# Kernel optimization log

Measured on AMD Instinct MI355X. Metric: run time of the kernel, lower is better.

## Reference

```python
import jax, jax.numpy as jnp
import numpy as np

N_NODES = 50000
N_EDGES = 1000000
IN_CH = 256
HID_CH = 128
HEADS = 2
OUT_CH = 3
NEG_SLOPE = 0.2  # PyG GATConv default leaky_relu slope


def setup_inputs() -> dict:
    key = jax.random.key(0)
    ks = jax.random.split(key, 10)
    s = 0.1
    x = jax.random.normal(ks[0], (N_NODES, IN_CH), dtype=jnp.float32)
    edge_index = jax.random.randint(ks[1], (2, N_EDGES), 0, N_NODES, dtype=jnp.int64)
    # GATConv layer 1 (heads=2, concat=True)
    W1 = jax.random.normal(ks[2], (IN_CH, HEADS * HID_CH), dtype=jnp.float32) * s
    a_src1 = jax.random.normal(ks[3], (HEADS, HID_CH), dtype=jnp.float32) * s
    a_dst1 = jax.random.normal(ks[4], (HEADS, HID_CH), dtype=jnp.float32) * s
    b1 = jnp.zeros((HEADS * HID_CH,), dtype=jnp.float32)
    # GATConv layer 2 (heads=1, concat=False)
    W2 = jax.random.normal(ks[5], (HEADS * HID_CH, OUT_CH), dtype=jnp.float32) * s
    a_src2 = jax.random.normal(ks[6], (1, OUT_CH), dtype=jnp.float32) * s
    a_dst2 = jax.random.normal(ks[7], (1, OUT_CH), dtype=jnp.float32) * s
    b2 = jnp.zeros((OUT_CH,), dtype=jnp.float32)
    return dict(x=x, edge_index=edge_index, W1=W1, a_src1=a_src1, a_dst1=a_dst1,
                b1=b1, W2=W2, a_src2=a_src2, a_dst2=a_dst2, b2=b2)


def gat_layer(x, edge_index, W, a_src, a_dst, b, concat):
    # x: [N, F_in]; W: [F_in, H*C]; a_src/a_dst: [H, C]
    n = x.shape[0]
    H, C = a_src.shape
    h = (x @ W).reshape(n, H, C)                       # [N, H, C]
    al_s = jnp.einsum('nhc,hc->nh', h, a_src)          # [N, H]
    al_d = jnp.einsum('nhc,hc->nh', h, a_dst)          # [N, H]
    src, dst = edge_index[0], edge_index[1]
    e = jax.nn.leaky_relu(al_s[src] + al_d[dst], NEG_SLOPE)   # [E, H]
    # segment softmax over incoming edges of each dst node
    e_max = jax.ops.segment_max(e, dst, num_segments=n)       # [N, H]
    w = jnp.exp(e - e_max[dst])                                # [E, H]
    denom = jax.ops.segment_sum(w, dst, num_segments=n)        # [N, H]
    alpha = w / jnp.maximum(denom[dst], 1e-16)                 # [E, H]
    out = jax.ops.segment_sum(h[src] * alpha[:, :, None], dst, num_segments=n)  # [N, H, C]
    out = out.reshape(n, H * C) if concat else out.mean(axis=1)
    return out + b


def reference(x, edge_index, W1, a_src1, a_dst1, b1, W2, a_src2, a_dst2, b2):
    # dropout(p=0.6) is identity in eval mode
    h = jax.nn.elu(gat_layer(x, edge_index, W1, a_src1, a_dst1, b1, concat=True))
    h = gat_layer(h, edge_index, W2, a_src2, a_dst2, b2, concat=False)
    return jax.nn.log_softmax(h, axis=1)
```

## Files before the change

### kernel.cpp

```cpp
#include <hip/hip_runtime.h>

#define N_NODES 50000
#define N_EDGES 1000000
#define FIN 256
#define F1  256
#define OUTC 3
#define BUCKET 64
#define GEMM_BLOCKS ((N_NODES + 63) / 64)
#define EDGE_BLOCKS ((N_EDGES + 255) / 256)

typedef __attribute__((ext_vector_type(8))) short  short8;
typedef __attribute__((ext_vector_type(4))) float  f32x4;
typedef __attribute__((ext_vector_type(2))) float  f32x2;

__device__ __forceinline__ unsigned short f2bf(float f) {
  unsigned int x; __builtin_memcpy(&x, &f, 4);
  x += 0x7fffu + ((x >> 16) & 1u);
  return (unsigned short)(x >> 16);
}
__device__ __forceinline__ float u2f(unsigned int x) {
  float f; __builtin_memcpy(&f, &x, 4); return f;
}
__device__ __forceinline__ float wredmax(float v) {
  #pragma unroll
  for (int m = 32; m > 0; m >>= 1) v = fmaxf(v, __shfl_xor(v, m));
  return v;
}
__device__ __forceinline__ float wredsum(float v) {
  #pragma unroll
  for (int m = 32; m > 0; m >>= 1) v += __shfl_xor(v, m);
  return v;
}

__global__ __launch_bounds__(256) void k_t(const float* __restrict__ w1,
                                           unsigned short* __restrict__ w1t,
                                           int* __restrict__ deg) {
  int idx = blockIdx.x * 256 + threadIdx.x;
  int k = idx >> 8, n = idx & 255;
  w1t[n * 256 + k] = f2bf(w1[k * 256 + n]);
  if (idx < N_NODES) deg[idx] = 0;
}

__global__ __launch_bounds__(256) void k_bg(
    const float* __restrict__ x,
    const unsigned short* __restrict__ w1t,
    const float* __restrict__ a_src1,
    const float* __restrict__ a_dst1,
    unsigned short* __restrict__ h1b,
    float* __restrict__ als1,
    float* __restrict__ ald1,
    const int* __restrict__ ei,
    int* __restrict__ deg, unsigned short* __restrict__ bucket) {
  const int t = threadIdx.x;

  if (blockIdx.x >= GEMM_BLOCKS) {
    __shared__ int sflag;
    if (t < 64) {
      int idx = 2 * (t * 15625 + 7) + 1;
      unsigned long long b = __ballot(ei[idx] != 0);
      if (t == 0) sflag = (b != 0ull) ? 1 : 0;
    }
    __syncthreads();
    const int f = sflag;
    int e = (blockIdx.x - GEMM_BLOCKS) * 256 + t;
    if (e < N_EDGES) {
      int s, d;
      if (f) { s = ei[e];     d = ei[N_EDGES + e]; }
      else   { s = ei[2 * e]; d = ei[2 * (N_EDGES + e)]; }
      int pos = atomicAdd(&deg[d], 1);
      if (pos < BUCKET) bucket[d * BUCKET + pos] = (unsigned short)s;
    }
    return;
  }

  const int wv   = t >> 6;
  const int lane = t & 63;
  const int m    = lane & 15;
  const int quad = lane >> 4;
  const int row0 = blockIdx.x * 64 + wv * 16;

  int arow = row0 + m;
  if (arow > N_NODES - 1) arow = N_NODES - 1;
  const float* xrow = x + (size_t)arow * FIN + quad * 8;

  short8 af[8];
  #pragma unroll
  for (int kk = 0; kk < 8; ++kk) {
    f32x4 v0 = *(const f32x4*)(xrow + kk * 32);
    f32x4 v1 = *(const f32x4*)(xrow + kk * 32 + 4);
    short8 fr;
    #pragma unroll
    for (int j = 0; j < 4; ++j) {
      fr[j]     = (short)f2bf(v0[j]);
      fr[j + 4] = (short)f2bf(v1[j]);
    }
    af[kk] = fr;
  }

  f32x4 acc[16];
  #pragma unroll
  for (int c = 0; c < 16; ++c) {
    const unsigned short* bp = w1t + (size_t)(c * 16 + m) * FIN + quad * 8;
    f32x4 a = {0.f, 0.f, 0.f, 0.f};
    #pragma unroll
    for (int kk = 0; kk < 8; ++kk) {
      short8 bf = *(const short8*)(bp + kk * 32);
      a = __builtin_amdgcn_mfma_f32_16x16x32_bf16(af[kk], bf, a, 0, 0, 0);
    }
    acc[c] = a;
  }

  float s0[4] = {0,0,0,0}, s1[4] = {0,0,0,0}, d0[4] = {0,0,0,0}, d1[4] = {0,0,0,0};
  #pragma unroll
  for (int c = 0; c < 16; ++c) {
    int ch = c * 16 + m;
    float av = a_src1[ch];
    float dv = a_dst1[ch];
    if (c < 8) {
      #pragma unroll
      for (int r = 0; r < 4; ++r) { s0[r] += acc[c][r] * av; d0[r] += acc[c][r] * dv; }
    } else {
      #pragma unroll
      for (int r = 0; r < 4; ++r) { s1[r] += acc[c][r] * av; d1[r] += acc[c][r] * dv; }
    }
  }
  #pragma unroll
  for (int msk = 1; msk < 16; msk <<= 1) {
    #pragma unroll
    for (int r = 0; r < 4; ++r) {
      s0[r] += __shfl_xor(s0[r], msk);
      s1[r] += __shfl_xor(s1[r], msk);
      d0[r] += __shfl_xor(d0[r], msk);
      d1[r] += __shfl_xor(d1[r], msk);
    }
  }
  #pragma unroll
  for (int r = 0; r < 4; ++r) {
    int row = row0 + quad * 4 + r;
    if (row < N_NODES) {
      unsigned short* hrow = h1b + (size_t)row * F1 + m;
      #pragma unroll
      for (int c = 0; c < 16; ++c) hrow[c * 16] = f2bf(acc[c][r]);
      if (m == 0) {
        als1[row * 2 + 0] = s0[r]; als1[row * 2 + 1] = s1[r];
        ald1[row * 2 + 0] = d0[r]; ald1[row * 2 + 1] = d1[r];
      }
    }
  }
}

__global__ __launch_bounds__(256) void k_attn1(
    const unsigned short* __restrict__ bucket,
    const int* __restrict__ deg,
    const float* __restrict__ als1,
    const float* __restrict__ ald1,
    const unsigned short* __restrict__ h1b,
    const float* __restrict__ b1,
    const float* __restrict__ w2,
    const float* __restrict__ a_src2,
    const float* __restrict__ a_dst2,
    float4* __restrict__ h2pack,
    float* __restrict__ ald2) {
  const int wv   = threadIdx.x >> 6;
  const int lane = threadIdx.x & 63;
  const int n = blockIdx.x * 4 + wv;
  if (n >= N_NODES) return;
  const int dg = min(deg[n], BUCKET);
  const float ad0  = ald1[n * 2 + 0];
  const float ad1v = ald1[n * 2 + 1];
  const float2* alsv = (const float2*)als1;

  const int l31   = lane & 31;
  const int ehalf = lane >> 5;
  const bool head1 = (l31 >= 16);

  float l0 = -1e30f, l1 = -1e30f; int sreg = 0;
  if (lane < dg) {
    sreg = (int)bucket[n * BUCKET + lane];
    float2 a = alsv[sreg];
    l0 = a.x + ad0;  l0 = l0 > 0.f ? l0 : 0.2f * l0;
    l1 = a.y + ad1v; l1 = l1 > 0.f ? l1 : 0.2f * l1;
  }
  const float m0 = wredmax(l0), m1 = wredmax(l1);
  const float e0 = (lane < dg) ? __expf(l0 - m0) : 0.f;
  const float e1 = (lane < dg) ? __expf(l1 - m1) : 0.f;
  const float sum0 = wredsum(e0), sum1 = wredsum(e1);
  const float inv = 1.f / fmaxf(head1 ? sum1 : sum0, 1e-16f);

  f32x2 accv[4] = {{0.f,0.f},{0.f,0.f},{0.f,0.f},{0.f,0.f}};
  const int pairs = (dg + 1) >> 1;
  for (int e = 0; e < pairs; e += 4) {
    float w[4]; int sv[4];
    #pragma unroll
    for (int k = 0; k < 4; ++k) {
      int eidx = 2 * (e + k) + ehalf;
      int esel = eidx & 63;
      float w0 = __shfl(e0, esel);
      float w1 = __shfl(e1, esel);
      sv[k] = __shfl(sreg, esel);
      w[k] = head1 ? w1 : w0;
      if (eidx >= dg) w[k] = 0.f;
    }
    uint4 hv[4];
    #pragma unroll
    for (int k = 0; k < 4; ++k)
      hv[k] = *(const uint4*)(h1b + (size_t)sv[k] * F1 + l31 * 8);
    #pragma unroll
    for (int k = 0; k < 4; ++k) {
      const unsigned int* hu = (const unsigned int*)&hv[k];
      f32x2 wv2 = {w[k], w[k]};
      #pragma unroll
      for (int j = 0; j < 4; ++j) {
        unsigned int u = hu[j];
        f32x2 h;
        h.x = u2f(u << 16);
        h.y = u2f(u & 0xffff0000u);
        accv[j] = __builtin_elementwise_fma(wv2, h, accv[j]);
      }
    }
  }

  float* av = (float*)accv;
  #pragma unroll
  for (int j = 0; j < 8; ++j) av[j] += __shfl_xor(av[j], 32);

  float p0 = 0.f, p1 = 0.f, p2 = 0.f;
  #pragma unroll
  for (int j = 0; j < 8; ++j) {
    int ch = l31 * 8 + j;
    float tt = av[j] * inv + b1[ch];
    tt = tt > 0.f ? tt : __expf(tt) - 1.f;
    p0 = fmaf(tt, w2[ch * 3 + 0], p0);
    p1 = fmaf(tt, w2[ch * 3 + 1], p1);
    p2 = fmaf(tt, w2[ch * 3 + 2], p2);
  }
  p0 = wredsum(p0) * 0.5f;
  p1 = wredsum(p1) * 0.5f;
  p2 = wredsum(p2) * 0.5f;
  if (lane == 0) {
    float als2v = p0 * a_src2[0] + p1 * a_src2[1] + p2 * a_src2[2];
    h2pack[n] = make_float4(p0, p1, p2, als2v);
    ald2[n] = p0 * a_dst2[0] + p1 * a_dst2[1] + p2 * a_dst2[2];
  }
}

__global__ __launch_bounds__(256) void k_attn2(
    const unsigned short* __restrict__ bucket,
    const int* __restrict__ deg,
    const float4* __restrict__ h2pack,
    const float* __restrict__ ald2,
    const float* __restrict__ b2,
    float* __restrict__ out) {
  const int wv   = threadIdx.x >> 6;
  const int lane = threadIdx.x & 63;
  const int n = blockIdx.x * 4 + wv;
  if (n >= N_NODES) return;
  const int dg = min(deg[n], BUCKET);
  const float adn = ald2[n];

  float l = -1e30f;
  float4 hp = make_float4(0.f, 0.f, 0.f, 0.f);
  if (lane < dg) {
    int s = (int)bucket[n * BUCKET + lane];
    hp = h2pack[s];
    l = hp.w + adn;
    l = l > 0.f ? l : 0.2f * l;
  }
  const float m = wredmax(l);
  const float e = (lane < dg) ? __expf(l - m) : 0.f;
  const float sum = wredsum(e);
  const float inv = 1.f / fmaxf(sum, 1e-16f);
  float p0 = wredsum(e * hp.x);
  float p1 = wredsum(e * hp.y);
  float p2 = wredsum(e * hp.z);

  if (lane == 0) {
    float o0 = p0 * inv + b2[0];
    float o1 = p1 * inv + b2[1];
    float o2 = p2 * inv + b2[2];
    float mm = fmaxf(o0, fmaxf(o1, o2));
    float ls = logf(__expf(o0 - mm) + __expf(o1 - mm) + __expf(o2 - mm));
    out[n * 3 + 0] = o0 - mm - ls;
    out[n * 3 + 1] = o1 - mm - ls;
    out[n * 3 + 2] = o2 - mm - ls;
  }
}

extern "C" void kernel_launch(void* const* d_in, const int* in_sizes, int n_in,
                              void* d_out, int out_size, void* d_ws, size_t ws_size,
                              hipStream_t stream) {
  (void)in_sizes; (void)n_in; (void)out_size; (void)ws_size;
  const float* x      = (const float*)d_in[0];
  const int*   ei     = (const int*)d_in[1];
  const float* W1     = (const float*)d_in[2];
  const float* a_src1 = (const float*)d_in[3];
  const float* a_dst1 = (const float*)d_in[4];
  const float* b1     = (const float*)d_in[5];
  const float* W2     = (const float*)d_in[6];
  const float* a_src2 = (const float*)d_in[7];
  const float* a_dst2 = (const float*)d_in[8];
  const float* b2     = (const float*)d_in[9];
  float* out = (float*)d_out;

  char* p = (char*)d_ws;
  auto alloc = [&](size_t bytes) -> char* {
    char* r = p; p += (bytes + 511) & ~(size_t)511; return r;
  };
  unsigned short* w1t  = (unsigned short*)alloc(65536ull * 2);
  unsigned short* h1b  = (unsigned short*)alloc((size_t)N_NODES * F1 * 2);
  float*  als1   = (float*)alloc((size_t)N_NODES * 2 * 4);
  float*  ald1   = (float*)alloc((size_t)N_NODES * 2 * 4);
  float4* h2pack = (float4*)alloc((size_t)N_NODES * 16);
  float*  ald2   = (float*)alloc((size_t)N_NODES * 4);
  int*    deg    = (int*)alloc((size_t)N_NODES * 4);
  unsigned short* bucket = (unsigned short*)alloc((size_t)N_NODES * BUCKET * 2);

  hipLaunchKernelGGL(k_t, dim3(256), dim3(256), 0, stream, W1, w1t, deg);
  hipLaunchKernelGGL(k_bg, dim3(GEMM_BLOCKS + EDGE_BLOCKS), dim3(256), 0, stream,
                     x, w1t, a_src1, a_dst1, h1b, als1, ald1, ei, deg, bucket);
  hipLaunchKernelGGL(k_attn1, dim3((N_NODES + 3) / 4), dim3(256), 0, stream,
                     bucket, deg, als1, ald1, h1b, b1, W2, a_src2, a_dst2,
                     h2pack, ald2);
  hipLaunchKernelGGL(k_attn2, dim3((N_NODES + 3) / 4), dim3(256), 0, stream,
                     bucket, deg, h2pack, ald2, b2, out);
}
```

Measured before the change: 252.8 us.

## Stage W1 slices in LDS per block and split GEMM by head

Drops the separate W1 transpose kernel. Each GEMM block now converts its own 128-column half of W1 to bf16 and stages it in shared memory in two K-chunks, then feeds the MFMAs from LDS instead of from global memory. The GEMM grid doubles so that each block handles one head, which halves the per-thread accumulators and the reduction work. The degree array is now zeroed with a memset. In exchange, every block re-reads and re-converts W1 from fp32 global memory and the x rows are loaded twice, adding redundant traffic and barriers.

```diff
diff --git a/kernel.cpp b/kernel.cpp
--- a/kernel.cpp
+++ b/kernel.cpp
@@ -6,8 +6,9 @@
 #define F1  256
 #define OUTC 3
 #define BUCKET 64
-#define GEMM_BLOCKS ((N_NODES + 63) / 64)
+#define GEMM_BLOCKS (((N_NODES + 63) / 64) * 2)
 #define EDGE_BLOCKS ((N_EDGES + 255) / 256)
+#define LDSW 136
 
 typedef __attribute__((ext_vector_type(8))) short  short8;
 typedef __attribute__((ext_vector_type(4))) float  f32x4;
@@ -32,18 +33,9 @@
   return v;
 }
 
-__global__ __launch_bounds__(256) void k_t(const float* __restrict__ w1,
-                                           unsigned short* __restrict__ w1t,
-                                           int* __restrict__ deg) {
-  int idx = blockIdx.x * 256 + threadIdx.x;
-  int k = idx >> 8, n = idx & 255;
-  w1t[n * 256 + k] = f2bf(w1[k * 256 + n]);
-  if (idx < N_NODES) deg[idx] = 0;
-}
-
-__global__ __launch_bounds__(256) void k_bg(
+__global__ __launch_bounds__(256) void k_bg2(
     const float* __restrict__ x,
-    const unsigned short* __restrict__ w1t,
+    const float* __restrict__ w1,
     const float* __restrict__ a_src1,
     const float* __restrict__ a_dst1,
     unsigned short* __restrict__ h1b,
@@ -51,6 +43,7 @@
     float* __restrict__ ald1,
     const int* __restrict__ ei,
     int* __restrict__ deg, unsigned short* __restrict__ bucket) {
+  __shared__ unsigned short lw[128 * LDSW];
   const int t = threadIdx.x;
 
   if (blockIdx.x >= GEMM_BLOCKS) {
@@ -73,11 +66,14 @@
     return;
   }
 
+  const int rb   = blockIdx.x >> 1;
+  const int s    = blockIdx.x & 1;
+  const int c0   = s * 128;
   const int wv   = t >> 6;
   const int lane = t & 63;
   const int m    = lane & 15;
   const int quad = lane >> 4;
-  const int row0 = blockIdx.x * 64 + wv * 16;
+  const int row0 = rb * 64 + wv * 16;
 
   int arow = row0 + m;
   if (arow > N_NODES - 1) arow = N_NODES - 1;
@@ -97,53 +93,63 @@
     af[kk] = fr;
   }
 
-  f32x4 acc[16];
-  #pragma unroll
-  for (int c = 0; c < 16; ++c) {
-    const unsigned short* bp = w1t + (size_t)(c * 16 + m) * FIN + quad * 8;
-    f32x4 a = {0.f, 0.f, 0.f, 0.f};
-    #pragma unroll
-    for (int kk = 0; kk < 8; ++kk) {
-      short8 bf = *(const short8*)(bp + kk * 32);
-      a = __builtin_amdgcn_mfma_f32_16x16x32_bf16(af[kk], bf, a, 0, 0, 0);
-    }
-    acc[c] = a;
-  }
-
-  float s0[4] = {0,0,0,0}, s1[4] = {0,0,0,0}, d0[4] = {0,0,0,0}, d1[4] = {0,0,0,0};
-  #pragma unroll
-  for (int c = 0; c < 16; ++c) {
-    int ch = c * 16 + m;
+  const int sc = t & 127;
+  const int sk = t >> 7;
+
+  f32x4 acc[8];
+  #pragma unroll
+  for (int c = 0; c < 8; ++c) acc[c] = (f32x4){0.f, 0.f, 0.f, 0.f};
+
+  #pragma unroll
+  for (int p = 0; p < 2; ++p) {
+    __syncthreads();
+    #pragma unroll 8
+    for (int i = 0; i < 64; ++i) {
+      int kl = sk + 2 * i;
+      lw[sc * LDSW + kl] = f2bf(w1[(size_t)(p * 128 + kl) * 256 + c0 + sc]);
+    }
+    __syncthreads();
+
+    #pragma unroll
+    for (int c = 0; c < 8; ++c) {
+      const unsigned short* bp = lw + (c * 16 + m) * LDSW + quad * 8;
+      f32x4 a = acc[c];
+      #pragma unroll
+      for (int kkl = 0; kkl < 4; ++kkl) {
+        short8 bf = *(const short8*)(bp + kkl * 32);
+        a = __builtin_amdgcn_mfma_f32_16x16x32_bf16(af[p * 4 + kkl], bf, a, 0, 0, 0);
+      }
+      acc[c] = a;
+    }
+  }
+
+  float sv[4] = {0,0,0,0}, dv[4] = {0,0,0,0};
+  #pragma unroll
+  for (int c = 0; c < 8; ++c) {
+    int ch = c0 + c * 16 + m;
     float av = a_src1[ch];
-    float dv = a_dst1[ch];
-    if (c < 8) {
-      #pragma unroll
-      for (int r = 0; r < 4; ++r) { s0[r] += acc[c][r] * av; d0[r] += acc[c][r] * dv; }
-    } else {
-      #pragma unroll
-      for (int r = 0; r < 4; ++r) { s1[r] += acc[c][r] * av; d1[r] += acc[c][r] * dv; }
-    }
+    float dvv = a_dst1[ch];
+    #pragma unroll
+    for (int r = 0; r < 4; ++r) { sv[r] += acc[c][r] * av; dv[r] += acc[c][r] * dvv; }
   }
   #pragma unroll
   for (int msk = 1; msk < 16; msk <<= 1) {
     #pragma unroll
     for (int r = 0; r < 4; ++r) {
-      s0[r] += __shfl_xor(s0[r], msk);
-      s1[r] += __shfl_xor(s1[r], msk);
-      d0[r] += __shfl_xor(d0[r], msk);
-      d1[r] += __shfl_xor(d1[r], msk);
+      sv[r] += __shfl_xor(sv[r], msk);
+      dv[r] += __shfl_xor(dv[r], msk);
     }
   }
   #pragma unroll
   for (int r = 0; r < 4; ++r) {
     int row = row0 + quad * 4 + r;
     if (row < N_NODES) {
-      unsigned short* hrow = h1b + (size_t)row * F1 + m;
+      unsigned short* hrow = h1b + (size_t)row * F1 + c0 + m;
       #pragma unroll
-      for (int c = 0; c < 16; ++c) hrow[c * 16] = f2bf(acc[c][r]);
+      for (int c = 0; c < 8; ++c) hrow[c * 16] = f2bf(acc[c][r]);
       if (m == 0) {
-        als1[row * 2 + 0] = s0[r]; als1[row * 2 + 1] = s1[r];
-        ald1[row * 2 + 0] = d0[r]; ald1[row * 2 + 1] = d1[r];
+        als1[row * 2 + s] = sv[r];
+        ald1[row * 2 + s] = dv[r];
       }
     }
   }
@@ -190,21 +196,21 @@
   f32x2 accv[4] = {{0.f,0.f},{0.f,0.f},{0.f,0.f},{0.f,0.f}};
   const int pairs = (dg + 1) >> 1;
   for (int e = 0; e < pairs; e += 4) {
-    float w[4]; int sv[4];
+    float w[4]; int svv[4];
     #pragma unroll
     for (int k = 0; k < 4; ++k) {
       int eidx = 2 * (e + k) + ehalf;
       int esel = eidx & 63;
       float w0 = __shfl(e0, esel);
       float w1 = __shfl(e1, esel);
-      sv[k] = __shfl(sreg, esel);
+      svv[k] = __shfl(sreg, esel);
       w[k] = head1 ? w1 : w0;
       if (eidx >= dg) w[k] = 0.f;
     }
     uint4 hv[4];
     #pragma unroll
     for (int k = 0; k < 4; ++k)
-      hv[k] = *(const uint4*)(h1b + (size_t)sv[k] * F1 + l31 * 8);
+      hv[k] = *(const uint4*)(h1b + (size_t)svv[k] * F1 + l31 * 8);
     #pragma unroll
     for (int k = 0; k < 4; ++k) {
       const unsigned int* hu = (const unsigned int*)&hv[k];
@@ -306,7 +312,6 @@
   auto alloc = [&](size_t bytes) -> char* {
     char* r = p; p += (bytes + 511) & ~(size_t)511; return r;
   };
-  unsigned short* w1t  = (unsigned short*)alloc(65536ull * 2);
   unsigned short* h1b  = (unsigned short*)alloc((size_t)N_NODES * F1 * 2);
   float*  als1   = (float*)alloc((size_t)N_NODES * 2 * 4);
   float*  ald1   = (float*)alloc((size_t)N_NODES * 2 * 4);
@@ -315,9 +320,9 @@
   int*    deg    = (int*)alloc((size_t)N_NODES * 4);
   unsigned short* bucket = (unsigned short*)alloc((size_t)N_NODES * BUCKET * 2);
 
-  hipLaunchKernelGGL(k_t, dim3(256), dim3(256), 0, stream, W1, w1t, deg);
-  hipLaunchKernelGGL(k_bg, dim3(GEMM_BLOCKS + EDGE_BLOCKS), dim3(256), 0, stream,
-                     x, w1t, a_src1, a_dst1, h1b, als1, ald1, ei, deg, bucket);
+  hipMemsetAsync(deg, 0, (size_t)N_NODES * 4, stream);
+  hipLaunchKernelGGL(k_bg2, dim3(GEMM_BLOCKS + EDGE_BLOCKS), dim3(256), 0, stream,
+                     x, W1, a_src1, a_dst1, h1b, als1, ald1, ei, deg, bucket);
   hipLaunchKernelGGL(k_attn1, dim3((N_NODES + 3) / 4), dim3(256), 0, stream,
                      bucket, deg, als1, ald1, h1b, b1, W2, a_src2, a_dst2,
                      h2pack, ald2);
```

After: 298.4 us. +18.0%, slower.
